# Kernel optimization log

Measured on AMD Instinct MI355X. Metric: run time of the kernel, lower is better.

## Reference

```python
import jax, jax.numpy as jnp
import numpy as np
import math

B, LQ, S, D = 8, 4096, 77, 1024
H, HD = 16, 64
R, ALPHA = 192, 16.0
LORA_SCALE = ALPHA / R
N_SUBJ = 32


def setup_inputs() -> dict:
    key = jax.random.key(0)
    ks = jax.random.split(key, 16)
    w = 0.02
    return {
        "hidden_states": jax.random.normal(ks[0], (B, LQ, D), jnp.float32),
        "encoder_hidden_states": jax.random.normal(ks[1], (B, S, D), jnp.float32),
        "Wq": jax.random.normal(ks[2], (D, D), jnp.float32) * w,
        "Wk": jax.random.normal(ks[3], (D, D), jnp.float32) * w,
        "Wv": jax.random.normal(ks[4], (D, D), jnp.float32) * w,
        "Wo": jax.random.normal(ks[5], (D, D), jnp.float32) * w,
        "bo": jnp.zeros((D,), jnp.float32),
        "Ak": jax.random.normal(ks[6], (R, D), jnp.float32) * w,
        "Bk": jax.random.normal(ks[7], (D, R), jnp.float32) * w,
        "Av": jax.random.normal(ks[8], (R, D), jnp.float32) * w,
        "Bv": jax.random.normal(ks[9], (D, R), jnp.float32) * w,
        "Ao": jax.random.normal(ks[10], (R, D), jnp.float32) * w,
        "Bo": jax.random.normal(ks[11], (D, R), jnp.float32) * w,
        "cross_attn_scale_factor": jnp.ones((), jnp.float32),
        "subj_b": jax.random.randint(ks[12], (N_SUBJ,), 0, B, jnp.int32),
        "subj_n": jax.random.randint(ks[13], (N_SUBJ,), 0, S, jnp.int32),
    }


def _lora(x, A, Bm):
    # peft LoRA delta: scale * (x @ A^T) @ B^T
    return LORA_SCALE * ((x @ A.T) @ Bm.T)


def reference(hidden_states, encoder_hidden_states, Wq, Wk, Wv, Wo, bo,
              Ak, Bk, Av, Bv, Ao, Bo, cross_attn_scale_factor, subj_b, subj_n):
    hs, ehs = hidden_states, encoder_hidden_states
    # q_lora_updates_query=False -> query uses the base projection only
    q = hs @ Wq.T                                  # [B, LQ, D]
    k = ehs @ Wk.T + _lora(ehs, Ak, Bk)            # [B, S, D] (to_k_lora)
    v = ehs @ Wv.T + _lora(ehs, Av, Bv)            # [B, S, D] (to_v_lora)

    q = q.reshape(B, LQ, H, HD).transpose(0, 2, 1, 3)   # [B,H,LQ,HD]
    k = k.reshape(B, S, H, HD).transpose(0, 2, 1, 3)    # [B,H,S,HD]
    v = v.reshape(B, S, H, HD).transpose(0, 2, 1, 3)

    scale = 1.0 / math.sqrt(HD)
    attn_score = jnp.einsum('bhld,bhsd->bhls', q, k) * scale  # [B,H,LQ,S]

    # normalize_cross_attn: zero-center subject-token scores over query dim,
    # then rescale by the learned cross_attn_scale_factor.
    sub = attn_score[subj_b, :, :, subj_n]                    # [K,H,LQ]
    sub = (sub - sub.mean(axis=2, keepdims=True)) * cross_attn_scale_factor
    attn_score = attn_score.at[subj_b, :, :, subj_n].set(sub)

    attn_weight = jax.nn.softmax(attn_score, axis=-1)
    out = jnp.einsum('bhls,bhsd->bhld', attn_weight, v)       # [B,H,LQ,HD]
    out = out.transpose(0, 2, 1, 3).reshape(B, LQ, D)

    # to_out_lora: base out-proj (with bias) + LoRA delta; to_out[1] dropout = id
    out = out @ Wo.T + bo + _lora(out, Ao, Bo)
    return out
```

## Files before the change

kernel.cpp:

```cpp
#include <hip/hip_runtime.h>
#include <stdint.h>

#define B_     8
#define LQ_    4096
#define S_     77
#define SP_    80
#define D_     1024
#define H_     16
#define HD_    64
#define NC_    1280
#define NSUBJ_ 32

typedef __attribute__((ext_vector_type(4))) float  f4;
typedef __attribute__((ext_vector_type(8))) short  short8;
typedef __attribute__((ext_vector_type(8))) unsigned short us8;
typedef __attribute__((ext_vector_type(4))) unsigned short us4;

__device__ __forceinline__ unsigned short f2bf(float f) {
  union { float f; unsigned u; } x; x.f = f;
  unsigned r = x.u + 0x7FFFu + ((x.u >> 16) & 1u);
  return (unsigned short)(r >> 16);
}
__device__ __forceinline__ float bf2f(unsigned short v) {
  union { unsigned u; float f; } x; x.u = ((unsigned)v) << 16;
  return x.f;
}

__device__ __forceinline__ void gload16(const void* g, void* s) {
  __builtin_amdgcn_global_load_lds((const __attribute__((address_space(1))) void*)g,
                                   (__attribute__((address_space(3))) void*)s, 16, 0, 0);
}

__global__ __launch_bounds__(256) void k_hssum(const float* __restrict__ hs,
                                               float* __restrict__ part,
                                               unsigned short* __restrict__ hsb) {
  int b = blockIdx.y;
  size_t base = ((size_t)b * LQ_ + (size_t)blockIdx.x * 64) * D_ + threadIdx.x * 4;
  f4 acc = {0.f, 0.f, 0.f, 0.f};
  for (int l = 0; l < 64; ++l) {
    f4 v = *(const f4*)(hs + base + (size_t)l * D_);
    acc += v;
    if (hsb) {
      us4 o;
#pragma unroll
      for (int j = 0; j < 4; ++j) o[j] = f2bf(v[j]);
      *(us4*)(hsb + base + (size_t)l * D_) = o;
    }
  }
  *(f4*)(part + (size_t)blockIdx.x * (B_ * D_) + b * D_ + threadIdx.x * 4) = acc;
}

__global__ __launch_bounds__(256) void k_hsred(const float* __restrict__ part,
                                               float* __restrict__ hssum) {
  int i = blockIdx.x * 256 + threadIdx.x;
  float s = 0.f;
  for (int x = 0; x < 64; ++x) s += part[(size_t)x * (B_ * D_) + i];
  hssum[i] = s;
}

__global__ __launch_bounds__(256) void k_prep(
    const float* __restrict__ Wq, const float* __restrict__ Ak,
    const float* __restrict__ Av, const float* __restrict__ Ao,
    const float* __restrict__ ehs,
    const float* __restrict__ Bk, const float* __restrict__ Bv, const float* __restrict__ Bo,
    unsigned short* __restrict__ wqTb, unsigned short* __restrict__ aTb,
    unsigned short* __restrict__ ehsb, unsigned short* __restrict__ bxb) {
  int z = blockIdx.z;
  int t = threadIdx.x;
  if (z == 4) {
    if (blockIdx.y >= 20) return;
    int gr = blockIdx.y * 32 + (t >> 3);
    int col = blockIdx.x * 32 + (t & 7) * 4;
    int b = gr / SP_, s = gr - b * SP_;
    us4 o = {0, 0, 0, 0};
    if (s < S_) {
      f4 v = *(const f4*)(ehs + ((size_t)b * S_ + s) * D_ + col);
#pragma unroll
      for (int j = 0; j < 4; ++j) o[j] = f2bf(v[j]);
    }
    *(us4*)(ehsb + (size_t)gr * D_ + col) = o;
    return;
  }
  if (z >= 5) {
    if (blockIdx.x >= 6) return;
    const float* in = z == 5 ? Bk : (z == 6 ? Bv : Bo);
    unsigned short* outp = bxb + (size_t)(z - 5) * 1024 * 192;
    int rr = blockIdx.y * 32 + (t >> 3);
    int c = blockIdx.x * 32 + (t & 7) * 4;
    f4 v = *(const f4*)(in + (size_t)rr * 192 + c);
    us4 o;
#pragma unroll
    for (int j = 0; j < 4; ++j) o[j] = f2bf(v[j]);
    *(us4*)(outp + (size_t)rr * 192 + c) = o;
    return;
  }
  const float* in = z == 0 ? Wq : (z == 1 ? Ak : (z == 2 ? Av : Ao));
  int R = z == 0 ? 1024 : 192;
  int c0 = blockIdx.x * 32, r0 = blockIdx.y * 32;
  if (r0 >= R) return;
  __shared__ float tile[32][33];
  int tx = t & 31, ty = t >> 5;
#pragma unroll
  for (int k = 0; k < 4; ++k)
    tile[ty + 8 * k][tx] = in[(size_t)(r0 + ty + 8 * k) * 1024 + c0 + tx];
  __syncthreads();
  unsigned short* outp = z == 0 ? wqTb : (aTb + (size_t)(z - 1) * 1024 * 192);
#pragma unroll
  for (int k = 0; k < 4; ++k)
    outp[(size_t)(c0 + ty + 8 * k) * R + r0 + tx] = f2bf(tile[tx][ty + 8 * k]);
}

__global__ __launch_bounds__(256) void k_weff_big(
    const unsigned short* __restrict__ bxb, const unsigned short* __restrict__ aTb,
    const float* __restrict__ Wk, const float* __restrict__ Wv, const float* __restrict__ Wo,
    unsigned short* __restrict__ wEb, float alpha) {
  __shared__ short As[128 * 64];
  __shared__ short Bs[128 * 64];
  int z = blockIdx.z;
  const unsigned short* Ab = bxb + (size_t)z * 1024 * 192;
  const unsigned short* Bb = aTb + (size_t)z * 1024 * 192;
  const float* Dm = z == 0 ? Wk : (z == 1 ? Wv : Wo);
  int m0 = blockIdx.x * 128, n0 = blockIdx.y * 128;
  int t = threadIdx.x, lane = t & 63, w = t >> 6;
  int wm = w >> 1, wn = w & 1;
  int r = lane & 15, q = lane >> 4;
  f4 acc[4][4] = {};

  for (int k0 = 0; k0 < 192; k0 += 64) {
    __syncthreads();
#pragma unroll
    for (int p = 0; p < 8; ++p) {
      int cb = p * 256 + w * 64;
      int cc = cb + lane;
      if (cb < 1024) {
        int row = cc >> 3, gc = (cc & 7) ^ (row & 7);
        gload16(Ab + (size_t)(m0 + row) * 192 + k0 + gc * 8, (char*)As + cb * 16);
      } else {
        int bc = cc - 1024, row = bc >> 3, gc = (bc & 7) ^ (row & 7);
        gload16(Bb + (size_t)(n0 + row) * 192 + k0 + gc * 8, (char*)Bs + (cb - 1024) * 16);
      }
    }
    __syncthreads();
#pragma unroll
    for (int kk = 0; kk < 2; ++kk) {
      short8 fa[4], fb[4];
#pragma unroll
      for (int mi = 0; mi < 4; ++mi) {
        int row = wm * 64 + mi * 16 + r;
        fa[mi] = *(const short8*)(As + row * 64 + (((kk * 4 + q) ^ (row & 7)) * 8));
      }
#pragma unroll
      for (int ni = 0; ni < 4; ++ni) {
        int row = wn * 64 + ni * 16 + r;
        fb[ni] = *(const short8*)(Bs + row * 64 + (((kk * 4 + q) ^ (row & 7)) * 8));
      }
#pragma unroll
      for (int mi = 0; mi < 4; ++mi)
#pragma unroll
        for (int ni = 0; ni < 4; ++ni)
          acc[mi][ni] = __builtin_amdgcn_mfma_f32_16x16x32_bf16(fa[mi], fb[ni], acc[mi][ni], 0, 0, 0);
    }
  }
#pragma unroll
  for (int mi = 0; mi < 4; ++mi)
#pragma unroll
    for (int ni = 0; ni < 4; ++ni)
#pragma unroll
      for (int j = 0; j < 4; ++j) {
        int row = m0 + wm * 64 + mi * 16 + q * 4 + j;
        int col = n0 + wn * 64 + ni * 16 + r;
        float val = acc[mi][ni][j] * alpha + Dm[(size_t)row * 1024 + col];
        wEb[(size_t)z * 1048576 + (size_t)row * 1024 + col] = f2bf(val);
      }
}

__global__ __launch_bounds__(256) void k_kv(const unsigned short* __restrict__ ehsb,
                                            const unsigned short* __restrict__ wEb,
                                            unsigned short* __restrict__ kvb) {
  __shared__ short As[80 * 64];
  __shared__ short Bs[64 * 64];
  int b = blockIdx.x >> 5, nt = blockIdx.x & 31;
  int n0 = nt * 64;
  const unsigned short* Ab = ehsb + (size_t)b * SP_ * D_;
  int t = threadIdx.x, lane = t & 63, w = t >> 6;
  int r = lane & 15, q = lane >> 4;
  f4 acc[5] = {{0,0,0,0},{0,0,0,0},{0,0,0,0},{0,0,0,0},{0,0,0,0}};

  for (int k0 = 0; k0 < 1024; k0 += 64) {
    __syncthreads();
#pragma unroll
    for (int p = 0; p < 5; ++p) {
      int cb = p * 256 + w * 64;
      if (cb < 1152) {
        int cc = cb + lane;
        if (cb < 640) {
          int row = cc >> 3, gc = (cc & 7) ^ (row & 7);
          gload16(Ab + (size_t)row * D_ + k0 + gc * 8, (char*)As + cb * 16);
        } else {
          int bc = cc - 640, row = bc >> 3, gc = (bc & 7) ^ (row & 7);
          gload16(wEb + (size_t)(n0 + row) * D_ + k0 + gc * 8, (char*)Bs + (cb - 640) * 16);
        }
      }
    }
    __syncthreads();
#pragma unroll
    for (int kk = 0; kk < 2; ++kk) {
      short8 fa[5], fb;
      {
        int row = w * 16 + r;
        fb = *(const short8*)(Bs + row * 64 + (((kk * 4 + q) ^ (row & 7)) * 8));
      }
#pragma unroll
      for (int mi = 0; mi < 5; ++mi) {
        int row = mi * 16 + r;
        fa[mi] = *(const short8*)(As + row * 64 + (((kk * 4 + q) ^ (row & 7)) * 8));
      }
#pragma unroll
      for (int mi = 0; mi < 5; ++mi)
        acc[mi] = __builtin_amdgcn_mfma_f32_16x16x32_bf16(fa[mi], fb, acc[mi], 0, 0, 0);
    }
  }
#pragma unroll
  for (int mi = 0; mi < 5; ++mi)
#pragma unroll
    for (int j = 0; j < 4; ++j) {
      int s = mi * 16 + q * 4 + j;
      int col = n0 + w * 16 + r;
      kvb[((size_t)b * SP_ + s) * 2048 + col] = f2bf(acc[mi][j]);
    }
}

__global__ __launch_bounds__(512) void k_mtut(const unsigned short* __restrict__ kvb,
                                              const unsigned short* __restrict__ wqTb,
                                              const unsigned short* __restrict__ wEb,
                                              unsigned short* __restrict__ Mt,
                                              unsigned short* __restrict__ Ut) {
  __shared__ short Ss[80 * 64];
  __shared__ short Ls[256 * 64];
  int z = blockIdx.x;
  bool mt = z < 128;
  int zz = mt ? z : z - 128;
  int b = zz >> 4, h = zz & 15;
  const unsigned short* small_src = kvb + (size_t)b * SP_ * 2048 + (mt ? h * 64 : 1024 + h * 64);
  const unsigned short* large_src = mt ? (wqTb + h * 64) : (wEb + (size_t)2048 * 1024 + h * 64);
  int t = threadIdx.x, lane = t & 63, w = t >> 6;
  int r = lane & 15, q = lane >> 4;

#pragma unroll
  for (int p = 0; p < 2; ++p) {
    int cb = p * 512 + w * 64;
    if (cb < 640) {
      int cc = cb + lane, row = cc >> 3, gc = (cc & 7) ^ (row & 7);
      gload16(small_src + (size_t)row * 2048 + gc * 8, (char*)Ss + cb * 16);
    }
  }

  for (int mc = 0; mc < 4; ++mc) {
    __syncthreads();
#pragma unroll
    for (int p = 0; p < 4; ++p) {
      int cb = p * 512 + w * 64;
      int cc = cb + lane, row = cc >> 3, gc = (cc & 7) ^ (row & 7);
      gload16(large_src + (size_t)(mc * 256 + row) * 1024 + gc * 8, (char*)Ls + cb * 16);
    }
    __syncthreads();

    if (mt) {
      f4 acc[5][2] = {};
#pragma unroll
      for (int kk = 0; kk < 2; ++kk) {
        int co = ((kk * 4 + q) ^ (r & 7)) * 8;
        short8 fa[5], fb[2];
#pragma unroll
        for (int mi = 0; mi < 5; ++mi)
          fa[mi] = *(const short8*)(Ss + (mi * 16 + r) * 64 + co);
#pragma unroll
        for (int ni = 0; ni < 2; ++ni)
          fb[ni] = *(const short8*)(Ls + (w * 32 + ni * 16 + r) * 64 + co);
#pragma unroll
        for (int mi = 0; mi < 5; ++mi)
#pragma unroll
          for (int ni = 0; ni < 2; ++ni)
            acc[mi][ni] = __builtin_amdgcn_mfma_f32_16x16x32_bf16(fa[mi], fb[ni], acc[mi][ni], 0, 0, 0);
      }
#pragma unroll
      for (int mi = 0; mi < 5; ++mi)
#pragma unroll
        for (int ni = 0; ni < 2; ++ni)
#pragma unroll
          for (int j = 0; j < 4; ++j) {
            int s = mi * 16 + q * 4 + j;
            int e = mc * 256 + w * 32 + ni * 16 + r;
            Mt[((size_t)b * NC_ + h * SP_ + s) * 1024 + e] = f2bf(acc[mi][ni][j] * 0.125f);
          }
    } else {
      f4 acc[2][5] = {};
#pragma unroll
      for (int kk = 0; kk < 2; ++kk) {
        int co = ((kk * 4 + q) ^ (r & 7)) * 8;
        short8 fa[2], fb[5];
#pragma unroll
        for (int mi = 0; mi < 2; ++mi)
          fa[mi] = *(const short8*)(Ls + (w * 32 + mi * 16 + r) * 64 + co);
#pragma unroll
        for (int ni = 0; ni < 5; ++ni)
          fb[ni] = *(const short8*)(Ss + (ni * 16 + r) * 64 + co);
#pragma unroll
        for (int mi = 0; mi < 2; ++mi)
#pragma unroll
          for (int ni = 0; ni < 5; ++ni)
            acc[mi][ni] = __builtin_amdgcn_mfma_f32_16x16x32_bf16(fa[mi], fb[ni], acc[mi][ni], 0, 0, 0);
      }
#pragma unroll
      for (int mi = 0; mi < 2; ++mi)
#pragma unroll
        for (int ni = 0; ni < 5; ++ni)
#pragma unroll
          for (int j = 0; j < 4; ++j) {
            int e = mc * 256 + w * 32 + mi * 16 + q * 4 + j;
            int col = h * SP_ + ni * 16 + r;
            Ut[((size_t)b * D_ + e) * NC_ + col] = f2bf(acc[mi][ni][j]);
          }
    }
  }
}

__global__ void k_mubeta(const float* __restrict__ hssum, const float* __restrict__ Wq,
                         const unsigned short* __restrict__ kvb,
                         const int* __restrict__ sb, const int* __restrict__ sn,
                         const float* __restrict__ csf_p,
                         float* __restrict__ alphav, float* __restrict__ betav) {
  int h = blockIdx.x, b = blockIdx.y;
  int t = threadIdx.x;
  __shared__ float qp[64];
  {
    int hd = t >> 1, half = t & 1;
    const float* wr = Wq + (size_t)(h * 64 + hd) * D_ + half * 512;
    const float* hp = hssum + b * D_ + half * 512;
    float s = 0.f;
    for (int d = 0; d < 512; d += 4) {
      f4 w = *(const f4*)(wr + d);
      f4 x = *(const f4*)(hp + d);
      s += w[0] * x[0] + w[1] * x[1] + w[2] * x[2] + w[3] * x[3];
    }
    s += __shfl_xor(s, 1, 64);
    if (half == 0) qp[hd] = s * (1.f / 4096.f);
  }
  __syncthreads();
  int s = t;
  if (s >= SP_) return;
  const unsigned short* kp = kvb + ((size_t)(b * SP_ + s)) * 2048 + h * HD_;
  float mu = 0.f;
#pragma unroll
  for (int hd = 0; hd < HD_; hd += 4) {
    us4 kv = *(const us4*)(kp + hd);
#pragma unroll
    for (int j = 0; j < 4; ++j) mu += qp[hd + j] * bf2f(kv[j]);
  }
  mu *= 0.125f;
  bool subj = false;
  for (int i = 0; i < NSUBJ_; ++i) subj = subj || (sb[i] == b && sn[i] == s);
  float csf = *csf_p;
  int c = b * NC_ + h * SP_ + s;
  alphav[c] = subj ? csf : 1.f;
  betav[c] = (s >= S_) ? -1e30f : (subj ? -mu * csf : 0.f);
}

__global__ __launch_bounds__(512, 2) void k_score_big(
    const unsigned short* __restrict__ hsb, const unsigned short* __restrict__ Mt,
    const float* __restrict__ alphav, const float* __restrict__ betav,
    unsigned short* __restrict__ P) {
  extern __shared__ short lds[];
  int id = blockIdx.x;
  int x = id & 7, idp = id >> 3;
  int nt = idp & 3;
  int pid = (idp >> 2) * 8 + x;
  int b = pid >> 4, mt = pid & 15;
  int m0 = mt * 256, n0 = nt * 320;

  const unsigned short* Ab = hsb + (size_t)b * LQ_ * D_;
  const unsigned short* Bb = Mt + (size_t)b * NC_ * D_;
  const float* alp = alphav + b * NC_;
  const float* bet = betav + b * NC_;
  unsigned short* Pb = P + (size_t)b * LQ_ * NC_;

  int t = threadIdx.x, lane = t & 63, wid = t >> 6;
  int wm = wid >> 2, wn = wid & 3;
  int r = lane & 15, q = lane >> 4;
  f4 acc[8][5] = {};

  auto SA = [&](int bf, int k0, int p) {
    int cb = p * 512 + wid * 64;
    int cc = cb + lane;
    int row = cc >> 2, gc = (cc & 3) ^ ((row >> 1) & 3);
    gload16(Ab + (size_t)(m0 + row) * D_ + k0 + gc * 8, (char*)(lds + bf * 8192) + cb * 16);
  };
  auto SB = [&](int bf, int k0, int p) {
    int cb = p * 512 + wid * 64;
    int cc = cb + lane;
    int row = cc >> 2, gc = (cc & 3) ^ ((row >> 1) & 3);
    gload16(Bb + (size_t)(n0 + row) * D_ + k0 + gc * 8, (char*)(lds + 32768 + bf * 10240) + cb * 16);
  };
  auto SBx = [&](int bf, int k0) {
    if (wid < 4) {
      int cb = 1024 + wid * 64;
      int cc = cb + lane;
      int row = cc >> 2, gc = (cc & 3) ^ ((row >> 1) & 3);
      gload16(Bb + (size_t)(n0 + row) * D_ + k0 + gc * 8, (char*)(lds + 32768 + bf * 10240) + cb * 16);
    }
  };
  auto STAGE_P1 = [&](int h) { if (h < 32) { int bf = h & 3, k0 = h * 32; SA(bf, k0, 0); SA(bf, k0, 1); SB(bf, k0, 0); } };
  auto STAGE_P2 = [&](int h) { if (h < 32) { int bf = h & 3, k0 = h * 32; SB(bf, k0, 1); SBx(bf, k0); } };

  STAGE_P1(0); STAGE_P2(0);
  STAGE_P1(1); STAGE_P2(1);
  STAGE_P1(2); STAGE_P2(2);
  if (wid < 4) asm volatile("s_waitcnt vmcnt(10)" ::: "memory");
  else         asm volatile("s_waitcnt vmcnt(8)" ::: "memory");
  __builtin_amdgcn_s_barrier();

#pragma unroll 1
  for (int h = 0; h < 32; ++h) {
    int bf = h & 3;
    const short* Ar = lds + bf * 8192;
    const short* Br = lds + 32768 + bf * 10240;
    short8 fa[4], fb[5];

#pragma unroll
    for (int ni = 0; ni < 5; ++ni) {
      int row = wn * 80 + ni * 16 + r;
      fb[ni] = *(const short8*)(Br + row * 32 + ((q ^ ((row >> 1) & 3)) * 8));
    }
#pragma unroll
    for (int mi = 0; mi < 4; ++mi) {
      int row = wm * 128 + mi * 16 + r;
      fa[mi] = *(const short8*)(Ar + row * 32 + ((q ^ ((row >> 1) & 3)) * 8));
    }
    __builtin_amdgcn_sched_barrier(0);
    STAGE_P1(h + 3);
    __builtin_amdgcn_sched_barrier(0);
    __builtin_amdgcn_s_barrier();
    asm volatile("s_waitcnt lgkmcnt(0)");
    __builtin_amdgcn_s_setprio(1);
#pragma unroll
    for (int mi = 0; mi < 4; ++mi)
#pragma unroll
      for (int ni = 0; ni < 5; ++ni)
        acc[mi][ni] = __builtin_amdgcn_mfma_f32_16x16x32_bf16(fa[mi], fb[ni], acc[mi][ni], 0, 0, 0);
    __builtin_amdgcn_s_setprio(0);

#pragma unroll
    for (int mi = 0; mi < 4; ++mi) {
      int row = wm * 128 + (4 + mi) * 16 + r;
      fa[mi] = *(const short8*)(Ar + row * 32 + ((q ^ ((row >> 1) & 3)) * 8));
    }
    __builtin_amdgcn_sched_barrier(0);
    STAGE_P2(h + 3);
    __builtin_amdgcn_sched_barrier(0);
    __builtin_amdgcn_s_barrier();
    asm volatile("s_waitcnt lgkmcnt(0)");
    __builtin_amdgcn_s_setprio(1);
#pragma unroll
    for (int mi = 0; mi < 4; ++mi)
#pragma unroll
      for (int ni = 0; ni < 5; ++ni)
        acc[4 + mi][ni] = __builtin_amdgcn_mfma_f32_16x16x32_bf16(fa[mi], fb[ni], acc[4 + mi][ni], 0, 0, 0);
    __builtin_amdgcn_s_setprio(0);

    if (h <= 28) {
      if (wid < 4) asm volatile("s_waitcnt vmcnt(10)" ::: "memory");
      else         asm volatile("s_waitcnt vmcnt(8)" ::: "memory");
    } else if (h == 29) {
      if (wid < 4) asm volatile("s_waitcnt vmcnt(5)" ::: "memory");
      else         asm volatile("s_waitcnt vmcnt(4)" ::: "memory");
    } else if (h == 30) {
      asm volatile("s_waitcnt vmcnt(0)" ::: "memory");
    }
    if (h < 31) __builtin_amdgcn_s_barrier();
  }

  float al[5], be[5];
#pragma unroll
  for (int ni = 0; ni < 5; ++ni) {
    int cc = n0 + wn * 80 + ni * 16 + r;
    al[ni] = alp[cc]; be[ni] = bet[cc];
  }
#pragma unroll
  for (int mi = 0; mi < 8; ++mi) {
#pragma unroll
    for (int j = 0; j < 4; ++j) {
      float v[5];
      float m = -3.0e38f;
#pragma unroll
      for (int ni = 0; ni < 5; ++ni) { v[ni] = acc[mi][ni][j] * al[ni] + be[ni]; m = fmaxf(m, v[ni]); }
#pragma unroll
      for (int off = 1; off < 16; off <<= 1) m = fmaxf(m, __shfl_xor(m, off, 64));
      float ssum = 0.f;
#pragma unroll
      for (int ni = 0; ni < 5; ++ni) { v[ni] = __expf(v[ni] - m); ssum += v[ni]; }
#pragma unroll
      for (int off = 1; off < 16; off <<= 1) ssum += __shfl_xor(ssum, off, 64);
      float inv = 1.f / ssum;
      int row = m0 + wm * 128 + mi * 16 + q * 4 + j;
      size_t rb = (size_t)row * NC_ + n0 + wn * 80 + r;
#pragma unroll
      for (int ni = 0; ni < 5; ++ni)
        Pb[rb + ni * 16] = f2bf(v[ni] * inv);
    }
  }
}

__global__ __launch_bounds__(256) void k_score_f32(
    const float* __restrict__ hs, const unsigned short* __restrict__ Mt,
    const float* __restrict__ alphav, const float* __restrict__ betav,
    unsigned short* __restrict__ P) {
  int id = blockIdx.x;
  int x = id & 7, idp = id >> 3;
  int n_t = idp & 7;
  int pid = (idp >> 3) * 8 + x;
  int b = pid >> 5, m_t = pid & 31;
  int m0 = m_t * 128, n0 = n_t * 160;
  const float* Af = hs + (size_t)b * LQ_ * D_;
  const unsigned short* Bb = Mt + (size_t)b * NC_ * D_;
  const float* alp = alphav + b * NC_;
  const float* bet = betav + b * NC_;
  unsigned short* Pb = P + (size_t)b * LQ_ * NC_;
  __shared__ short As[128 * 64];
  __shared__ short Bs[160 * 64];
  int t = threadIdx.x, lane = t & 63, wid = t >> 6;
  int wm = wid >> 1, wn = wid & 1;
  int srow = lane >> 3;
  int schunk = (lane & 7) ^ srow;
  f4 acc[4][5] = {};
  for (int k0 = 0; k0 < D_; k0 += 64) {
    __syncthreads();
    for (int i = wid; i < 20; i += 4)
      gload16(Bb + (size_t)(n0 + i * 8 + srow) * D_ + k0 + schunk * 8, (char*)Bs + i * 1024);
    int arow = t >> 3, ac = t & 7;
    int awc = ac ^ (arow & 7);
#pragma unroll
    for (int p = 0; p < 4; ++p) {
      int row = p * 32 + arow;
      const float* src = Af + (size_t)(m0 + row) * D_ + k0 + ac * 8;
      f4 v0 = *(const f4*)src;
      f4 v1 = *(const f4*)(src + 4);
      us8 u;
#pragma unroll
      for (int j = 0; j < 4; ++j) { u[j] = f2bf(v0[j]); u[4 + j] = f2bf(v1[j]); }
      *(us8*)(As + row * 64 + awc * 8) = u;
    }
    __syncthreads();
#pragma unroll
    for (int kk = 0; kk < 2; ++kk) {
      int co = ((kk * 4 + (lane >> 4)) ^ (lane & 7)) * 8;
      short8 fa[4], fb[5];
#pragma unroll
      for (int mi = 0; mi < 4; ++mi)
        fa[mi] = *(const short8*)(As + (wm * 64 + mi * 16 + (lane & 15)) * 64 + co);
#pragma unroll
      for (int ni = 0; ni < 5; ++ni)
        fb[ni] = *(const short8*)(Bs + (wn * 80 + ni * 16 + (lane & 15)) * 64 + co);
#pragma unroll
      for (int mi = 0; mi < 4; ++mi)
#pragma unroll
        for (int ni = 0; ni < 5; ++ni)
          acc[mi][ni] = __builtin_amdgcn_mfma_f32_16x16x32_bf16(fa[mi], fb[ni], acc[mi][ni], 0, 0, 0);
    }
  }
  float al[5], be[5];
#pragma unroll
  for (int ni = 0; ni < 5; ++ni) {
    int cc = n0 + wn * 80 + ni * 16 + (lane & 15);
    al[ni] = alp[cc]; be[ni] = bet[cc];
  }
#pragma unroll
  for (int mi = 0; mi < 4; ++mi) {
#pragma unroll
    for (int j = 0; j < 4; ++j) {
      float v[5];
      float m = -3.0e38f;
#pragma unroll
      for (int ni = 0; ni < 5; ++ni) { v[ni] = acc[mi][ni][j] * al[ni] + be[ni]; m = fmaxf(m, v[ni]); }
#pragma unroll
      for (int off = 1; off < 16; off <<= 1) m = fmaxf(m, __shfl_xor(m, off, 64));
      float ssum = 0.f;
#pragma unroll
      for (int ni = 0; ni < 5; ++ni) { v[ni] = __expf(v[ni] - m); ssum += v[ni]; }
#pragma unroll
      for (int off = 1; off < 16; off <<= 1) ssum += __shfl_xor(ssum, off, 64);
      float inv = 1.f / ssum;
      int row = m0 + wm * 64 + mi * 16 + (lane >> 4) * 4 + j;
      size_t rb = (size_t)row * NC_ + n0 + wn * 80 + (lane & 15);
#pragma unroll
      for (int ni = 0; ni < 5; ++ni)
        Pb[rb + ni * 16] = f2bf(v[ni] * inv);
    }
  }
}

__global__ __launch_bounds__(512, 2) void k_out_big(
    const unsigned short* __restrict__ P, const unsigned short* __restrict__ Ut,
    const float* __restrict__ bo, float* __restrict__ out) {
  extern __shared__ short lds[];
  int id = blockIdx.x;
  int x = id & 7, idp = id >> 3;
  int nt = idp & 3;
  int pid = (idp >> 2) * 8 + x;
  int b = pid >> 4, mt = pid & 15;
  int m0 = mt * 256, n0 = nt * 256;

  const unsigned short* Ab = P + (size_t)b * LQ_ * NC_;
  const unsigned short* Bb = Ut + (size_t)b * D_ * NC_;
  float* ob = out + (size_t)b * LQ_ * D_;

  int t = threadIdx.x, lane = t & 63, wid = t >> 6;
  int wm = wid >> 2, wn = wid & 3;
  int r = lane & 15, q = lane >> 4;
  f4 acc[8][4] = {};
  const int T = NC_ / 32;

  auto SA = [&](int bf, int k0, int p) {
    int cb = p * 512 + wid * 64;
    int cc = cb + lane;
    int row = cc >> 2, gc = (cc & 3) ^ ((row >> 1) & 3);
    gload16(Ab + (size_t)(m0 + row) * NC_ + k0 + gc * 8, (char*)(lds + bf * 8192) + cb * 16);
  };
  auto SB = [&](int bf, int k0, int p) {
    int cb = p * 512 + wid * 64;
    int cc = cb + lane;
    int row = cc >> 2, gc = (cc & 3) ^ ((row >> 1) & 3);
    gload16(Bb + (size_t)(n0 + row) * NC_ + k0 + gc * 8, (char*)(lds + 32768 + bf * 8192) + cb * 16);
  };
  auto STAGE_P1 = [&](int h) { if (h < T) { int bf = h & 3, k0 = h * 32; SA(bf, k0, 0); SA(bf, k0, 1); } };
  auto STAGE_P2 = [&](int h) { if (h < T) { int bf = h & 3, k0 = h * 32; SB(bf, k0, 0); SB(bf, k0, 1); } };

  STAGE_P1(0); STAGE_P2(0);
  STAGE_P1(1); STAGE_P2(1);
  STAGE_P1(2); STAGE_P2(2);
  asm volatile("s_waitcnt vmcnt(8)" ::: "memory");
  __builtin_amdgcn_s_barrier();

#pragma unroll 1
  for (int h = 0; h < T; ++h) {
    int bf = h & 3;
    const short* Ar = lds + bf * 8192;
    const short* Br = lds + 32768 + bf * 8192;
    short8 fa[4], fb[4];

#pragma unroll
    for (int ni = 0; ni < 4; ++ni) {
      int row = wn * 64 + ni * 16 + r;
      fb[ni] = *(const short8*)(Br + row * 32 + ((q ^ ((row >> 1) & 3)) * 8));
    }
#pragma unroll
    for (int mi = 0; mi < 4; ++mi) {
      int row = wm * 128 + mi * 16 + r;
      fa[mi] = *(const short8*)(Ar + row * 32 + ((q ^ ((row >> 1) & 3)) * 8));
    }
    __builtin_amdgcn_sched_barrier(0);
    STAGE_P1(h + 3);
    __builtin_amdgcn_sched_barrier(0);
    __builtin_amdgcn_s_barrier();
    asm volatile("s_waitcnt lgkmcnt(0)");
    __builtin_amdgcn_s_setprio(1);
#pragma unroll
    for (int mi = 0; mi < 4; ++mi)
#pragma unroll
      for (int ni = 0; ni < 4; ++ni)
        acc[mi][ni] = __builtin_amdgcn_mfma_f32_16x16x32_bf16(fa[mi], fb[ni], acc[mi][ni], 0, 0, 0);
    __builtin_amdgcn_s_setprio(0);

#pragma unroll
    for (int mi = 0; mi < 4; ++mi) {
      int row = wm * 128 + (4 + mi) * 16 + r;
      fa[mi] = *(const short8*)(Ar + row * 32 + ((q ^ ((row >> 1) & 3)) * 8));
    }
    __builtin_amdgcn_sched_barrier(0);
    STAGE_P2(h + 3);
    __builtin_amdgcn_sched_barrier(0);
    __builtin_amdgcn_s_barrier();
    asm volatile("s_waitcnt lgkmcnt(0)");
    __builtin_amdgcn_s_setprio(1);
#pragma unroll
    for (int mi = 0; mi < 4; ++mi)
#pragma unroll
      for (int ni = 0; ni < 4; ++ni)
        acc[4 + mi][ni] = __builtin_amdgcn_mfma_f32_16x16x32_bf16(fa[mi], fb[ni], acc[4 + mi][ni], 0, 0, 0);
    __builtin_amdgcn_s_setprio(0);

    if (h <= T - 4) {
      asm volatile("s_waitcnt vmcnt(8)" ::: "memory");
    } else if (h == T - 3) {
      asm volatile("s_waitcnt vmcnt(4)" ::: "memory");
    } else if (h == T - 2) {
      asm volatile("s_waitcnt vmcnt(0)" ::: "memory");
    }
    if (h < T - 1) __builtin_amdgcn_s_barrier();
  }

#pragma unroll
  for (int ni = 0; ni < 4; ++ni) {
    int col = n0 + wn * 64 + ni * 16 + r;
    float bov = bo[col];
#pragma unroll
    for (int mi = 0; mi < 8; ++mi)
#pragma unroll
      for (int j = 0; j < 4; ++j) {
        int row = m0 + wm * 128 + mi * 16 + q * 4 + j;
        ob[(size_t)row * D_ + col] = acc[mi][ni][j] + bov;
      }
  }
}

extern "C" void kernel_launch(void* const* d_in, const int* in_sizes, int n_in,
                              void* d_out, int out_size, void* d_ws, size_t ws_size,
                              hipStream_t stream) {
  const float* hs  = (const float*)d_in[0];
  const float* ehs = (const float*)d_in[1];
  const float* Wq  = (const float*)d_in[2];
  const float* Wk  = (const float*)d_in[3];
  const float* Wv  = (const float*)d_in[4];
  const float* Wo  = (const float*)d_in[5];
  const float* bo  = (const float*)d_in[6];
  const float* Ak  = (const float*)d_in[7];
  const float* Bk  = (const float*)d_in[8];
  const float* Av  = (const float*)d_in[9];
  const float* Bv  = (const float*)d_in[10];
  const float* Ao  = (const float*)d_in[11];
  const float* Bo  = (const float*)d_in[12];
  const float* csf = (const float*)d_in[13];
  const int*   sb  = (const int*)d_in[14];
  const int*   sn  = (const int*)d_in[15];
  float* out = (float*)d_out;

  hipFuncSetAttribute(reinterpret_cast<const void*>(k_score_big),
                      hipFuncAttributeMaxDynamicSharedMemorySize, 147456);
  hipFuncSetAttribute(reinterpret_cast<const void*>(k_out_big),
                      hipFuncAttributeMaxDynamicSharedMemorySize, 131072);

  char* ws = (char*)d_ws;
  unsigned short* P  = (unsigned short*)ws;
  unsigned short* Mt = (unsigned short*)(ws + 83886080);
  unsigned short* Ut = (unsigned short*)(ws + 104857600);
  const size_t NEED_HSB = 125829120ULL + 67108864ULL + 81920ULL;
  bool useHsb = ws_size >= NEED_HSB;
  unsigned short* hsb = useHsb ? (unsigned short*)(ws + 125829120) : nullptr;
  char* tail = useHsb ? (ws + 192937984) : (ws + 125829120);
  float* alphav = (float*)tail;
  float* betav  = (float*)(tail + 40960);
  unsigned short* kvb   = (unsigned short*)(ws + 0);
  unsigned short* wEb   = (unsigned short*)(ws + 2621440);
  unsigned short* wqTb  = (unsigned short*)(ws + 8912896);
  unsigned short* aTb   = (unsigned short*)(ws + 11010048);
  unsigned short* bxb   = (unsigned short*)(ws + 12189696);
  unsigned short* ehsb  = (unsigned short*)(ws + 13369344);
  float*          part  = (float*)(ws + 14680064);
  float*          hssum = (float*)(ws + 16777216);

  const float LS = 16.0f / 192.0f;

  k_hssum<<<dim3(64, 8), 256, 0, stream>>>(hs, part, hsb);
  k_hsred<<<32, 256, 0, stream>>>(part, hssum);

  k_prep<<<dim3(32, 32, 8), 256, 0, stream>>>(Wq, Ak, Av, Ao, ehs, Bk, Bv, Bo,
                                              wqTb, aTb, ehsb, bxb);

  k_weff_big<<<dim3(8, 8, 3), 256, 0, stream>>>(bxb, aTb, Wk, Wv, Wo, wEb, LS);

  k_kv<<<256, 256, 0, stream>>>(ehsb, wEb, kvb);

  k_mtut<<<256, 512, 0, stream>>>(kvb, wqTb, wEb, Mt, Ut);

  k_mubeta<<<dim3(16, 8), 128, 0, stream>>>(hssum, Wq, kvb, sb, sn, csf, alphav, betav);

  if (useHsb)
    k_score_big<<<512, 512, 147456, stream>>>(hsb, Mt, alphav, betav, P);
  else
    k_score_f32<<<2048, 256, 0, stream>>>(hs, Mt, alphav, betav, P);
  k_out_big<<<512, 512, 131072, stream>>>(P, Ut, bo, out);

  (void)in_sizes; (void)n_in; (void)out_size; (void)ws_size;
}
```

Baseline: 331.1 us.

## Halve N tiles and switch GEMMs to a triple-buffered pipeline for higher occupancy

Both the score GEMM and the output GEMM now use half-width N tiles (160 and 128 columns) with a 4x2 wave grid, so each wave holds half as many accumulators. The grid doubles to 1024 blocks, and LDS per block shrinks to allow more resident blocks (launch bounds raised to 4). The hand-interleaved quad-buffer pipeline is replaced by a simpler triple-buffer loop that prefetches two stages ahead with a barrier per K step. The trade-off is more global reloads of the A tile across N tiles and less careful overlap of loads with MFMA work.

```diff
diff --git a/kernel.cpp b/kernel.cpp
--- a/kernel.cpp
+++ b/kernel.cpp
@@ -366,17 +366,20 @@
   betav[c] = (s >= S_) ? -1e30f : (subj ? -mu * csf : 0.f);
 }
 
-__global__ __launch_bounds__(512, 2) void k_score_big(
+__global__ __launch_bounds__(512, 4) void k_score_big(
     const unsigned short* __restrict__ hsb, const unsigned short* __restrict__ Mt,
     const float* __restrict__ alphav, const float* __restrict__ betav,
     unsigned short* __restrict__ P) {
   extern __shared__ short lds[];
+  const int ASZ = 8192;
+  const int BSZ = 5120;
+  short* B0 = lds + 3 * ASZ;
   int id = blockIdx.x;
   int x = id & 7, idp = id >> 3;
-  int nt = idp & 3;
-  int pid = (idp >> 2) * 8 + x;
+  int nt = idp & 7;
+  int pid = (idp >> 3) * 8 + x;
   int b = pid >> 4, mt = pid & 15;
-  int m0 = mt * 256, n0 = nt * 320;
+  int m0 = mt * 256, n0 = nt * 160;
 
   const unsigned short* Ab = hsb + (size_t)b * LQ_ * D_;
   const unsigned short* Bb = Mt + (size_t)b * NC_ * D_;
@@ -385,47 +388,51 @@
   unsigned short* Pb = P + (size_t)b * LQ_ * NC_;
 
   int t = threadIdx.x, lane = t & 63, wid = t >> 6;
-  int wm = wid >> 2, wn = wid & 3;
+  int wm = wid >> 1, wn = wid & 1;
   int r = lane & 15, q = lane >> 4;
-  f4 acc[8][5] = {};
-
-  auto SA = [&](int bf, int k0, int p) {
-    int cb = p * 512 + wid * 64;
-    int cc = cb + lane;
-    int row = cc >> 2, gc = (cc & 3) ^ ((row >> 1) & 3);
-    gload16(Ab + (size_t)(m0 + row) * D_ + k0 + gc * 8, (char*)(lds + bf * 8192) + cb * 16);
-  };
-  auto SB = [&](int bf, int k0, int p) {
-    int cb = p * 512 + wid * 64;
-    int cc = cb + lane;
-    int row = cc >> 2, gc = (cc & 3) ^ ((row >> 1) & 3);
-    gload16(Bb + (size_t)(n0 + row) * D_ + k0 + gc * 8, (char*)(lds + 32768 + bf * 10240) + cb * 16);
-  };
-  auto SBx = [&](int bf, int k0) {
-    if (wid < 4) {
-      int cb = 1024 + wid * 64;
+  f4 acc[4][5] = {};
+
+  auto STAGE = [&](int bf, int k0) {
+#pragma unroll
+    for (int p = 0; p < 2; ++p) {
+      int cb = p * 512 + wid * 64;
       int cc = cb + lane;
       int row = cc >> 2, gc = (cc & 3) ^ ((row >> 1) & 3);
-      gload16(Bb + (size_t)(n0 + row) * D_ + k0 + gc * 8, (char*)(lds + 32768 + bf * 10240) + cb * 16);
+      gload16(Ab + (size_t)(m0 + row) * D_ + k0 + gc * 8, (char*)(lds + bf * ASZ) + cb * 16);
+    }
+    {
+      int cb = wid * 64;
+      int cc = cb + lane;
+      int row = cc >> 2, gc = (cc & 3) ^ ((row >> 1) & 3);
+      gload16(Bb + (size_t)(n0 + row) * D_ + k0 + gc * 8, (char*)(B0 + bf * BSZ) + cb * 16);
+    }
+    if (wid < 2) {
+      int cb = 512 + wid * 64;
+      int cc = cb + lane;
+      int row = cc >> 2, gc = (cc & 3) ^ ((row >> 1) & 3);
+      gload16(Bb + (size_t)(n0 + row) * D_ + k0 + gc * 8, (char*)(B0 + bf * BSZ) + cb * 16);
     }
   };
-  auto STAGE_P1 = [&](int h) { if (h < 32) { int bf = h & 3, k0 = h * 32; SA(bf, k0, 0); SA(bf, k0, 1); SB(bf, k0, 0); } };
-  auto STAGE_P2 = [&](int h) { if (h < 32) { int bf = h & 3, k0 = h * 32; SB(bf, k0, 1); SBx(bf, k0); } };
-
-  STAGE_P1(0); STAGE_P2(0);
-  STAGE_P1(1); STAGE_P2(1);
-  STAGE_P1(2); STAGE_P2(2);
-  if (wid < 4) asm volatile("s_waitcnt vmcnt(10)" ::: "memory");
-  else         asm volatile("s_waitcnt vmcnt(8)" ::: "memory");
-  __builtin_amdgcn_s_barrier();
-
-#pragma unroll 1
-  for (int h = 0; h < 32; ++h) {
-    int bf = h & 3;
-    const short* Ar = lds + bf * 8192;
-    const short* Br = lds + 32768 + bf * 10240;
+
+  const int T = 32;
+  STAGE(0, 0); STAGE(1, 32);
+  for (int h = 0; h < T; ++h) {
+    int bf = h - (h / 3) * 3;
+    if (h + 2 < T) {
+      int h2 = h + 2, bf2 = h2 - (h2 / 3) * 3;
+      STAGE(bf2, h2 * 32);
+      if (wid < 2) asm volatile("s_waitcnt vmcnt(8)" ::: "memory");
+      else         asm volatile("s_waitcnt vmcnt(6)" ::: "memory");
+    } else if (h + 1 < T) {
+      if (wid < 2) asm volatile("s_waitcnt vmcnt(4)" ::: "memory");
+      else         asm volatile("s_waitcnt vmcnt(3)" ::: "memory");
+    } else {
+      asm volatile("s_waitcnt vmcnt(0)" ::: "memory");
+    }
+    __builtin_amdgcn_s_barrier();
+    const short* Ar = lds + bf * ASZ;
+    const short* Br = B0 + bf * BSZ;
     short8 fa[4], fb[5];
-
 #pragma unroll
     for (int ni = 0; ni < 5; ++ni) {
       int row = wn * 80 + ni * 16 + r;
@@ -433,14 +440,9 @@
     }
 #pragma unroll
     for (int mi = 0; mi < 4; ++mi) {
-      int row = wm * 128 + mi * 16 + r;
+      int row = wm * 64 + mi * 16 + r;
       fa[mi] = *(const short8*)(Ar + row * 32 + ((q ^ ((row >> 1) & 3)) * 8));
     }
-    __builtin_amdgcn_sched_barrier(0);
-    STAGE_P1(h + 3);
-    __builtin_amdgcn_sched_barrier(0);
-    __builtin_amdgcn_s_barrier();
-    asm volatile("s_waitcnt lgkmcnt(0)");
     __builtin_amdgcn_s_setprio(1);
 #pragma unroll
     for (int mi = 0; mi < 4; ++mi)
@@ -448,35 +450,7 @@
       for (int ni = 0; ni < 5; ++ni)
         acc[mi][ni] = __builtin_amdgcn_mfma_f32_16x16x32_bf16(fa[mi], fb[ni], acc[mi][ni], 0, 0, 0);
     __builtin_amdgcn_s_setprio(0);
-
-#pragma unroll
-    for (int mi = 0; mi < 4; ++mi) {
-      int row = wm * 128 + (4 + mi) * 16 + r;
-      fa[mi] = *(const short8*)(Ar + row * 32 + ((q ^ ((row >> 1) & 3)) * 8));
-    }
-    __builtin_amdgcn_sched_barrier(0);
-    STAGE_P2(h + 3);
-    __builtin_amdgcn_sched_barrier(0);
     __builtin_amdgcn_s_barrier();
-    asm volatile("s_waitcnt lgkmcnt(0)");
-    __builtin_amdgcn_s_setprio(1);
-#pragma unroll
-    for (int mi = 0; mi < 4; ++mi)
-#pragma unroll
-      for (int ni = 0; ni < 5; ++ni)
-        acc[4 + mi][ni] = __builtin_amdgcn_mfma_f32_16x16x32_bf16(fa[mi], fb[ni], acc[4 + mi][ni], 0, 0, 0);
-    __builtin_amdgcn_s_setprio(0);
-
-    if (h <= 28) {
-      if (wid < 4) asm volatile("s_waitcnt vmcnt(10)" ::: "memory");
-      else         asm volatile("s_waitcnt vmcnt(8)" ::: "memory");
-    } else if (h == 29) {
-      if (wid < 4) asm volatile("s_waitcnt vmcnt(5)" ::: "memory");
-      else         asm volatile("s_waitcnt vmcnt(4)" ::: "memory");
-    } else if (h == 30) {
-      asm volatile("s_waitcnt vmcnt(0)" ::: "memory");
-    }
-    if (h < 31) __builtin_amdgcn_s_barrier();
   }
 
   float al[5], be[5];
@@ -486,7 +460,7 @@
     al[ni] = alp[cc]; be[ni] = bet[cc];
   }
 #pragma unroll
-  for (int mi = 0; mi < 8; ++mi) {
+  for (int mi = 0; mi < 4; ++mi) {
 #pragma unroll
     for (int j = 0; j < 4; ++j) {
       float v[5];
@@ -501,7 +475,7 @@
 #pragma unroll
       for (int off = 1; off < 16; off <<= 1) ssum += __shfl_xor(ssum, off, 64);
       float inv = 1.f / ssum;
-      int row = m0 + wm * 128 + mi * 16 + q * 4 + j;
+      int row = m0 + wm * 64 + mi * 16 + q * 4 + j;
       size_t rb = (size_t)row * NC_ + n0 + wn * 80 + r;
 #pragma unroll
       for (int ni = 0; ni < 5; ++ni)
@@ -598,55 +572,62 @@
   }
 }
 
-__global__ __launch_bounds__(512, 2) void k_out_big(
+__global__ __launch_bounds__(512, 4) void k_out_big(
     const unsigned short* __restrict__ P, const unsigned short* __restrict__ Ut,
     const float* __restrict__ bo, float* __restrict__ out) {
   extern __shared__ short lds[];
+  const int ASZ = 8192;
+  const int BSZ = 4096;
+  short* B0 = lds + 3 * ASZ;
   int id = blockIdx.x;
   int x = id & 7, idp = id >> 3;
-  int nt = idp & 3;
-  int pid = (idp >> 2) * 8 + x;
+  int nt = idp & 7;
+  int pid = (idp >> 3) * 8 + x;
   int b = pid >> 4, mt = pid & 15;
-  int m0 = mt * 256, n0 = nt * 256;
+  int m0 = mt * 256, n0 = nt * 128;
 
   const unsigned short* Ab = P + (size_t)b * LQ_ * NC_;
   const unsigned short* Bb = Ut + (size_t)b * D_ * NC_;
   float* ob = out + (size_t)b * LQ_ * D_;
 
   int t = threadIdx.x, lane = t & 63, wid = t >> 6;
-  int wm = wid >> 2, wn = wid & 3;
+  int wm = wid >> 1, wn = wid & 1;
   int r = lane & 15, q = lane >> 4;
-  f4 acc[8][4] = {};
+  f4 acc[4][4] = {};
   const int T = NC_ / 32;
 
-  auto SA = [&](int bf, int k0, int p) {
-    int cb = p * 512 + wid * 64;
-    int cc = cb + lane;
-    int row = cc >> 2, gc = (cc & 3) ^ ((row >> 1) & 3);
-    gload16(Ab + (size_t)(m0 + row) * NC_ + k0 + gc * 8, (char*)(lds + bf * 8192) + cb * 16);
+  auto STAGE = [&](int bf, int k0) {
+#pragma unroll
+    for (int p = 0; p < 2; ++p) {
+      int cb = p * 512 + wid * 64;
+      int cc = cb + lane;
+      int row = cc >> 2, gc = (cc & 3) ^ ((row >> 1) & 3);
+      gload16(Ab + (size_t)(m0 + row) * NC_ + k0 + gc * 8, (char*)(lds + bf * ASZ) + cb * 16);
+    }
+    {
+      int cb = wid * 64;
+      int cc = cb + lane;
+      int row = cc >> 2, gc = (cc & 3) ^ ((row >> 1) & 3);
+      gload16(Bb + (size_t)(n0 + row) * NC_ + k0 + gc * 8, (char*)(B0 + bf * BSZ) + cb * 16);
+    }
   };
-  auto SB = [&](int bf, int k0, int p) {
-    int cb = p * 512 + wid * 64;
-    int cc = cb + lane;
-    int row = cc >> 2, gc = (cc & 3) ^ ((row >> 1) & 3);
-    gload16(Bb + (size_t)(n0 + row) * NC_ + k0 + gc * 8, (char*)(lds + 32768 + bf * 8192) + cb * 16);
-  };
-  auto STAGE_P1 = [&](int h) { if (h < T) { int bf = h & 3, k0 = h * 32; SA(bf, k0, 0); SA(bf, k0, 1); } };
-  auto STAGE_P2 = [&](int h) { if (h < T) { int bf = h & 3, k0 = h * 32; SB(bf, k0, 0); SB(bf, k0, 1); } };
-
-  STAGE_P1(0); STAGE_P2(0);
-  STAGE_P1(1); STAGE_P2(1);
-  STAGE_P1(2); STAGE_P2(2);
-  asm volatile("s_waitcnt vmcnt(8)" ::: "memory");
-  __builtin_amdgcn_s_barrier();
-
-#pragma unroll 1
+
+  STAGE(0, 0); STAGE(1, 32);
   for (int h = 0; h < T; ++h) {
-    int bf = h & 3;
-    const short* Ar = lds + bf * 8192;
-    const short* Br = lds + 32768 + bf * 8192;
+    int bf = h - (h / 3) * 3;
+    if (h + 2 < T) {
+      int h2 = h + 2, bf2 = h2 - (h2 / 3) * 3;
+      STAGE(bf2, h2 * 32);
+      asm volatile("s_waitcnt vmcnt(6)" ::: "memory");
+    } else if (h + 1 < T) {
+      asm volatile("s_waitcnt vmcnt(3)" ::: "memory");
+    } else {
+      asm volatile("s_waitcnt vmcnt(0)" ::: "memory");
+    }
+    __builtin_amdgcn_s_barrier();
+    const short* Ar = lds + bf * ASZ;
+    const short* Br = B0 + bf * BSZ;
     short8 fa[4], fb[4];
-
 #pragma unroll
     for (int ni = 0; ni < 4; ++ni) {
       int row = wn * 64 + ni * 16 + r;
@@ -654,14 +635,9 @@
     }
 #pragma unroll
     for (int mi = 0; mi < 4; ++mi) {
-      int row = wm * 128 + mi * 16 + r;
+      int row = wm * 64 + mi * 16 + r;
       fa[mi] = *(const short8*)(Ar + row * 32 + ((q ^ ((row >> 1) & 3)) * 8));
     }
-    __builtin_amdgcn_sched_barrier(0);
-    STAGE_P1(h + 3);
-    __builtin_amdgcn_sched_barrier(0);
-    __builtin_amdgcn_s_barrier();
-    asm volatile("s_waitcnt lgkmcnt(0)");
     __builtin_amdgcn_s_setprio(1);
 #pragma unroll
     for (int mi = 0; mi < 4; ++mi)
@@ -669,33 +645,7 @@
       for (int ni = 0; ni < 4; ++ni)
         acc[mi][ni] = __builtin_amdgcn_mfma_f32_16x16x32_bf16(fa[mi], fb[ni], acc[mi][ni], 0, 0, 0);
     __builtin_amdgcn_s_setprio(0);
-
-#pragma unroll
-    for (int mi = 0; mi < 4; ++mi) {
-      int row = wm * 128 + (4 + mi) * 16 + r;
-      fa[mi] = *(const short8*)(Ar + row * 32 + ((q ^ ((row >> 1) & 3)) * 8));
-    }
-    __builtin_amdgcn_sched_barrier(0);
-    STAGE_P2(h + 3);
-    __builtin_amdgcn_sched_barrier(0);
     __builtin_amdgcn_s_barrier();
-    asm volatile("s_waitcnt lgkmcnt(0)");
-    __builtin_amdgcn_s_setprio(1);
-#pragma unroll
-    for (int mi = 0; mi < 4; ++mi)
-#pragma unroll
-      for (int ni = 0; ni < 4; ++ni)
-        acc[4 + mi][ni] = __builtin_amdgcn_mfma_f32_16x16x32_bf16(fa[mi], fb[ni], acc[4 + mi][ni], 0, 0, 0);
-    __builtin_amdgcn_s_setprio(0);
-
-    if (h <= T - 4) {
-      asm volatile("s_waitcnt vmcnt(8)" ::: "memory");
-    } else if (h == T - 3) {
-      asm volatile("s_waitcnt vmcnt(4)" ::: "memory");
-    } else if (h == T - 2) {
-      asm volatile("s_waitcnt vmcnt(0)" ::: "memory");
-    }
-    if (h < T - 1) __builtin_amdgcn_s_barrier();
   }
 
 #pragma unroll
@@ -703,10 +653,10 @@
     int col = n0 + wn * 64 + ni * 16 + r;
     float bov = bo[col];
 #pragma unroll
-    for (int mi = 0; mi < 8; ++mi)
+    for (int mi = 0; mi < 4; ++mi)
 #pragma unroll
       for (int j = 0; j < 4; ++j) {
-        int row = m0 + wm * 128 + mi * 16 + q * 4 + j;
+        int row = m0 + wm * 64 + mi * 16 + q * 4 + j;
         ob[(size_t)row * D_ + col] = acc[mi][ni][j] + bov;
       }
   }
@@ -734,9 +684,9 @@
   float* out = (float*)d_out;
 
   hipFuncSetAttribute(reinterpret_cast<const void*>(k_score_big),
-                      hipFuncAttributeMaxDynamicSharedMemorySize, 147456);
+                      hipFuncAttributeMaxDynamicSharedMemorySize, 79872);
   hipFuncSetAttribute(reinterpret_cast<const void*>(k_out_big),
-                      hipFuncAttributeMaxDynamicSharedMemorySize, 131072);
+                      hipFuncAttributeMaxDynamicSharedMemorySize, 73728);
 
   char* ws = (char*)d_ws;
   unsigned short* P  = (unsigned short*)ws;
@@ -774,10 +724,10 @@
   k_mubeta<<<dim3(16, 8), 128, 0, stream>>>(hssum, Wq, kvb, sb, sn, csf, alphav, betav);
 
   if (useHsb)
-    k_score_big<<<512, 512, 147456, stream>>>(hsb, Mt, alphav, betav, P);
+    k_score_big<<<1024, 512, 79872, stream>>>(hsb, Mt, alphav, betav, P);
   else
     k_score_f32<<<2048, 256, 0, stream>>>(hs, Mt, alphav, betav, P);
-  k_out_big<<<512, 512, 131072, stream>>>(P, Ut, bo, out);
+  k_out_big<<<1024, 512, 73728, stream>>>(P, Ut, bo, out);
 
   (void)in_sizes; (void)n_in; (void)out_size; (void)ws_size;
 }
```

After: 361.6 us. 9.2% more time.
